# Kernel optimization log

Hardware: AMD Instinct MI355X
Metric: run time of the kernel (lower is better)

Reference implementation:

```python
import jax, jax.numpy as jnp
import numpy as np

B, S, D, H = 4, 2048, 768, 12
DEPTH = D // H


def setup_inputs() -> dict:
    key = jax.random.key(0)
    ks = jax.random.split(key, 8)
    scale = 1.0 / np.sqrt(D)
    return {
        "v": jax.random.normal(ks[0], (B, S, D), jnp.float32),
        "k": jax.random.normal(ks[1], (B, S, D), jnp.float32),
        "q": jax.random.normal(ks[2], (B, S, D), jnp.float32),
        "wq": jax.random.normal(ks[3], (D, D), jnp.float32) * scale,
        "wk": jax.random.normal(ks[4], (D, D), jnp.float32) * scale,
        "wv": jax.random.normal(ks[5], (D, D), jnp.float32) * scale,
        "wo": jax.random.normal(ks[6], (D, D), jnp.float32) * scale,
        "bo": jax.random.normal(ks[7], (D,), jnp.float32) * 0.01,
    }


def _split_heads(x):
    # [B, S, D] -> [B, H, S, depth]
    return x.reshape(B, S, H, DEPTH).transpose(0, 2, 1, 3)


def reference(v, k, q, wq, wk, wv, wo, bo):
    # nn.Linear(bias=False): y = x @ W.T
    qh = _split_heads(q @ wq.T)
    kh = _split_heads(k @ wk.T)
    vh = _split_heads(v @ wv.T)
    # scaled dot-product attention (mask=None)
    logits = jnp.einsum("bhqd,bhkd->bhqk", qh, kh) / jnp.sqrt(
        jnp.asarray(DEPTH, jnp.float32)
    )
    attn = jax.nn.softmax(logits, axis=-1)  # [B, H, Sq, Sk]
    out = jnp.einsum("bhqk,bhkd->bhqd", attn, vh)
    concat = out.transpose(0, 2, 1, 3).reshape(B, S, D)
    return concat @ wo.T + bo
```

## Files before the change

### kernel.cpp

```cpp
#include <hip/hip_runtime.h>
#include <math.h>

#define BB 4
#define SS 2048
#define DD 768
#define HH 12
#define DEPTH 64
#define M_TOTAL (BB * SS)
#define WSZ (DD * DD)

typedef __attribute__((ext_vector_type(8))) short bf16x8;
typedef __attribute__((ext_vector_type(16))) float f32x16;
typedef __attribute__((ext_vector_type(4))) float f32x4;
typedef __attribute__((ext_vector_type(4))) unsigned short us4;

__device__ __forceinline__ unsigned short f2b(float f) {
  union { float f; unsigned int u; } v;
  v.f = f;
  unsigned int u = v.u;
  return (unsigned short)((u + 0x7FFFu + ((u >> 16) & 1u)) >> 16);
}

__device__ __forceinline__ us4 f2b4(float a, float b, float c, float d) {
  us4 t;
  t.x = f2b(a); t.y = f2b(b); t.z = f2b(c); t.w = f2b(d);
  return t;
}

__device__ __forceinline__ float fexp2(float x) {
  return __builtin_amdgcn_exp2f(x);
}

__device__ __forceinline__ void gl16(const void* g, void* l) {
  __builtin_amdgcn_global_load_lds(
      (const __attribute__((address_space(1))) unsigned int*)g,
      (__attribute__((address_space(3))) unsigned int*)l, 16, 0, 0);
}

__global__ __launch_bounds__(256) void prep(
    const float* __restrict__ s0, const float* __restrict__ s1,
    const float* __restrict__ s2, const float* __restrict__ s3,
    const float* __restrict__ s4, const float* __restrict__ s5,
    const float* __restrict__ s6, unsigned short* __restrict__ d0,
    unsigned short* __restrict__ d1, unsigned short* __restrict__ d2,
    unsigned short* __restrict__ d3, unsigned short* __restrict__ d4,
    unsigned short* __restrict__ d5, unsigned short* __restrict__ d6) {
  const float* s;
  unsigned short* d;
  int n;
  switch (blockIdx.y) {
    case 0: s = s0; d = d0; n = M_TOTAL * DD; break;
    case 1: s = s1; d = d1; n = M_TOTAL * DD; break;
    case 2: s = s2; d = d2; n = M_TOTAL * DD; break;
    case 3: s = s3; d = d3; n = WSZ; break;
    case 4: s = s4; d = d4; n = WSZ; break;
    case 5: s = s5; d = d5; n = WSZ; break;
    default: s = s6; d = d6; n = WSZ; break;
  }
  int idx = (blockIdx.x * 256 + threadIdx.x) * 4;
  if (idx >= n) return;
  float4 f = *(const float4*)(s + idx);
  *(us4*)(d + idx) = f2b4(f.x, f.y, f.z, f.w);
}

__global__ __launch_bounds__(256) void proj_qkv(
    const unsigned short* __restrict__ qb, const unsigned short* __restrict__ kb,
    const unsigned short* __restrict__ vb, const unsigned short* __restrict__ wqb,
    const unsigned short* __restrict__ wkb, const unsigned short* __restrict__ wvb,
    unsigned short* __restrict__ QF, unsigned short* __restrict__ KF,
    unsigned short* __restrict__ VF) {
  const int mode = blockIdx.z;
  const unsigned short* X;
  const unsigned short* W;
  if (mode == 0) { X = qb; W = wqb; }
  else if (mode == 1) { X = kb; W = wkb; }
  else { X = vb; W = wvb; }

  __shared__ __align__(16) unsigned short As[128 * 32];
  __shared__ __align__(16) unsigned short Bs[128 * 32];

  const int tid = threadIdx.x;
  const int lane = tid & 63, w_ = tid >> 6;
  const int lr = lane & 15, quad = lane >> 4;
  const int wm = (w_ & 1) * 64, wn = (w_ >> 1) * 64;
  const int m0 = blockIdx.x * 128, n0 = blockIdx.y * 128;
  const int grow = lane >> 2, gcol = (lane & 3) * 8;

  f32x4 acc[4][4];
#pragma unroll
  for (int mt = 0; mt < 4; ++mt)
#pragma unroll
    for (int nt = 0; nt < 4; ++nt) acc[mt][nt] = (f32x4){0.f, 0.f, 0.f, 0.f};

  for (int k0 = 0; k0 < DD; k0 += 32) {
    __syncthreads();
#pragma unroll
    for (int i = 0; i < 2; ++i) {
      int c = 4 * i + w_;
      int row = c * 16 + grow;
      gl16(X + (size_t)(m0 + row) * DD + k0 + gcol, (char*)As + c * 1024);
      gl16(W + (size_t)(n0 + row) * DD + k0 + gcol, (char*)Bs + c * 1024);
    }
    __syncthreads();

    bf16x8 af[4];
#pragma unroll
    for (int mt = 0; mt < 4; ++mt)
      af[mt] = *(const bf16x8*)&As[(wm + 16 * mt + lr) * 32 + 8 * quad];
#pragma unroll
    for (int nt = 0; nt < 4; ++nt) {
      bf16x8 bf = *(const bf16x8*)&Bs[(wn + 16 * nt + lr) * 32 + 8 * quad];
#pragma unroll
      for (int mt = 0; mt < 4; ++mt)
        acc[mt][nt] = __builtin_amdgcn_mfma_f32_16x16x32_bf16(af[mt], bf,
                                                              acc[mt][nt], 0, 0, 0);
    }
  }

  if (mode < 2) {
    unsigned short* O = (mode == 0) ? QF : KF;
    const float osc = (mode == 0) ? 0.18033688011f : 1.0f;
#pragma unroll
    for (int mt = 0; mt < 4; ++mt)
#pragma unroll
      for (int nt = 0; nt < 4; ++nt) {
        int n = n0 + wn + 16 * nt + lr;
        int head = n >> 6, d = n & 63;
        int ks = d >> 4, hbit = (d >> 3) & 1, j = d & 7;
#pragma unroll
        for (int r = 0; r < 4; ++r) {
          int m = m0 + wm + 16 * mt + 4 * quad + r;
          int b_ = m >> 11, s_ = m & 2047;
          int bh = b_ * HH + head;
          int lane2 = hbit * 32 + (s_ & 31);
          size_t off =
              ((((size_t)bh * 64 + (s_ >> 5)) * 4 + ks) * 64 + lane2) * 8 + j;
          O[off] = f2b(acc[mt][nt][r] * osc);
        }
      }
  } else {
#pragma unroll
    for (int mt = 0; mt < 4; ++mt)
#pragma unroll
      for (int nt = 0; nt < 4; ++nt) {
        int n = n0 + wn + 16 * nt + lr;
        int head = n >> 6, d = n & 63;
        int ntv = d >> 5, m32v = d & 31;
        int mb = m0 + wm + 16 * mt + 4 * quad;
        int b_ = mb >> 11, s_ = mb & 2047;
        int bh = b_ * HH + head;
        int sblk = s_ >> 5, ks2 = (s_ >> 4) & 1, hb = (s_ >> 3) & 1, jb = s_ & 7;
        int lane2 = hb * 32 + m32v;
        size_t off =
            (((((size_t)bh * 64 + sblk) * 2 + ntv) * 2 + ks2) * 64 + lane2) * 8 +
            jb;
        *(us4*)&VF[off] =
            f2b4(acc[mt][nt][0], acc[mt][nt][1], acc[mt][nt][2], acc[mt][nt][3]);
      }
  }
}

__global__ __launch_bounds__(256) void attn(
    const unsigned short* __restrict__ QF, const unsigned short* __restrict__ KF,
    const unsigned short* __restrict__ VF, unsigned short* __restrict__ cc) {
  __shared__ __align__(16) char smem[19200];
  unsigned short (*Ps)[32][40] = (unsigned short (*)[32][40])smem;
  float (*Osh)[64][36] = (float (*)[64][36])smem;
  float (*Ls)[2][32] = (float (*)[2][32])(smem + 18432);
  float (*Linv)[32] = (float (*)[32])(smem + 18944);

  const int tid = threadIdx.x;
  const int lane = tid & 63, w_ = tid >> 6;
  const int wq = w_ & 1, wk = w_ >> 1;
  const int m32 = lane & 31, h = lane >> 5;
  const int q0 = blockIdx.x * 64;
  const int bh = blockIdx.y;
  const size_t perbh = (size_t)SS * DEPTH;

  const unsigned short* qfb = QF + (size_t)bh * perbh;
  const unsigned short* kfb = KF + (size_t)bh * perbh;
  const unsigned short* vfb = VF + (size_t)bh * perbh;

  bf16x8 qf[4];
  {
    const int qblk = (q0 >> 5) + wq;
    const unsigned short* p = qfb + (size_t)qblk * 2048 + lane * 8;
#pragma unroll
    for (int ks = 0; ks < 4; ++ks) qf[ks] = *(const bf16x8*)(p + ks * 512);
  }

  f32x16 o[2];
#pragma unroll
  for (int nt = 0; nt < 2; ++nt)
#pragma unroll
    for (int r = 0; r < 16; ++r) o[nt][r] = 0.f;
  float l_lane = 0.f;

  bf16x8 ka[4], vf[4];
  {
    const int sb = wk;
    const unsigned short* kp = kfb + (size_t)sb * 2048 + lane * 8;
    const unsigned short* vp = vfb + (size_t)sb * 2048 + lane * 8;
#pragma unroll
    for (int x = 0; x < 4; ++x) {
      ka[x] = *(const bf16x8*)(kp + x * 512);
      vf[x] = *(const bf16x8*)(vp + x * 512);
    }
  }

  for (int kv0 = 0; kv0 < SS; kv0 += 64) {
    bf16x8 kan[4], vfn[4];
    const bool more = (kv0 + 64 < SS);
    if (more) {
      const int sb = ((kv0 + 64) >> 5) + wk;
      const unsigned short* kp = kfb + (size_t)sb * 2048 + lane * 8;
      const unsigned short* vp = vfb + (size_t)sb * 2048 + lane * 8;
#pragma unroll
      for (int x = 0; x < 4; ++x) {
        kan[x] = *(const bf16x8*)(kp + x * 512);
        vfn[x] = *(const bf16x8*)(vp + x * 512);
      }
    }

    f32x16 st;
#pragma unroll
    for (int r = 0; r < 16; ++r) st[r] = 0.f;
#pragma unroll
    for (int ks = 0; ks < 4; ++ks)
      st = __builtin_amdgcn_mfma_f32_32x32x16_bf16(ka[ks], qf[ks], st, 0, 0, 0);

#pragma unroll
    for (int g = 0; g < 4; ++g) {
      float e0 = fexp2(st[4 * g + 0]);
      float e1 = fexp2(st[4 * g + 1]);
      float e2 = fexp2(st[4 * g + 2]);
      float e3 = fexp2(st[4 * g + 3]);
      l_lane += (e0 + e1) + (e2 + e3);
      *(us4*)&Ps[w_][m32][8 * g + 4 * h] = f2b4(e0, e1, e2, e3);
    }
    asm volatile("s_waitcnt lgkmcnt(0)" ::: "memory");

#pragma unroll
    for (int ks2 = 0; ks2 < 2; ++ks2) {
      bf16x8 pa = *(const bf16x8*)&Ps[w_][m32][16 * ks2 + 8 * h];
      o[0] = __builtin_amdgcn_mfma_f32_32x32x16_bf16(pa, vf[ks2], o[0], 0, 0, 0);
      o[1] = __builtin_amdgcn_mfma_f32_32x32x16_bf16(pa, vf[2 + ks2], o[1], 0, 0, 0);
    }

    if (more) {
#pragma unroll
      for (int x = 0; x < 4; ++x) { ka[x] = kan[x]; vf[x] = vfn[x]; }
    }
  }

  l_lane += __shfl_xor(l_lane, 32);
  if (h == 0) Ls[wq][wk][m32] = l_lane;
  __syncthreads();
  if (wk == 1) {
#pragma unroll
    for (int nt = 0; nt < 2; ++nt)
#pragma unroll
      for (int g = 0; g < 4; ++g) {
        float4 t = make_float4(o[nt][4 * g], o[nt][4 * g + 1], o[nt][4 * g + 2],
                               o[nt][4 * g + 3]);
        *(float4*)&Osh[wq][32 * nt + m32][8 * g + 4 * h] = t;
      }
  } else if (tid < 64) {
    int qq = tid & 31, ww = tid >> 5;
    Linv[ww][qq] = 1.f / (Ls[ww][0][qq] + Ls[ww][1][qq]);
  }
  __syncthreads();
  if (wk == 0) {
    const int b_ = bh / HH, h_ = bh % HH;
#pragma unroll
    for (int g = 0; g < 4; ++g) {
      float4 li = *(const float4*)&Linv[wq][8 * g + 4 * h];
      float lia[4] = {li.x, li.y, li.z, li.w};
#pragma unroll
      for (int nt = 0; nt < 2; ++nt) {
        float4 ot = *(const float4*)&Osh[wq][32 * nt + m32][8 * g + 4 * h];
        float oa[4] = {ot.x, ot.y, ot.z, ot.w};
#pragma unroll
        for (int r = 0; r < 4; ++r) {
          int qg = q0 + 32 * wq + 8 * g + 4 * h + r;
          float val = (o[nt][4 * g + r] + oa[r]) * lia[r];
          cc[((size_t)b_ * SS + qg) * DD + h_ * DEPTH + 32 * nt + m32] = f2b(val);
        }
      }
    }
  }
}

__global__ __launch_bounds__(256) void proj_out(
    const unsigned short* __restrict__ cc, const unsigned short* __restrict__ wob,
    const float* __restrict__ bo, float* __restrict__ out) {
  __shared__ __align__(16) unsigned short As[128 * 32];
  __shared__ __align__(16) unsigned short Bs[128 * 32];

  const int tid = threadIdx.x;
  const int lane = tid & 63, w_ = tid >> 6;
  const int lr = lane & 15, quad = lane >> 4;
  const int wm = (w_ & 1) * 64, wn = (w_ >> 1) * 64;
  const int m0 = blockIdx.x * 128, n0 = blockIdx.y * 128;
  const int grow = lane >> 2, gcol = (lane & 3) * 8;

  f32x4 acc[4][4];
#pragma unroll
  for (int mt = 0; mt < 4; ++mt)
#pragma unroll
    for (int nt = 0; nt < 4; ++nt) acc[mt][nt] = (f32x4){0.f, 0.f, 0.f, 0.f};

  for (int k0 = 0; k0 < DD; k0 += 32) {
    __syncthreads();
#pragma unroll
    for (int i = 0; i < 2; ++i) {
      int c = 4 * i + w_;
      int row = c * 16 + grow;
      gl16(cc + (size_t)(m0 + row) * DD + k0 + gcol, (char*)As + c * 1024);
      gl16(wob + (size_t)(n0 + row) * DD + k0 + gcol, (char*)Bs + c * 1024);
    }
    __syncthreads();

    bf16x8 af[4];
#pragma unroll
    for (int mt = 0; mt < 4; ++mt)
      af[mt] = *(const bf16x8*)&As[(wm + 16 * mt + lr) * 32 + 8 * quad];
#pragma unroll
    for (int nt = 0; nt < 4; ++nt) {
      bf16x8 bf = *(const bf16x8*)&Bs[(wn + 16 * nt + lr) * 32 + 8 * quad];
#pragma unroll
      for (int mt = 0; mt < 4; ++mt)
        acc[mt][nt] = __builtin_amdgcn_mfma_f32_16x16x32_bf16(af[mt], bf,
                                                              acc[mt][nt], 0, 0, 0);
    }
  }

#pragma unroll
  for (int mt = 0; mt < 4; ++mt)
#pragma unroll
    for (int nt = 0; nt < 4; ++nt) {
      int n = n0 + wn + 16 * nt + lr;
      float bias = bo[n];
#pragma unroll
      for (int r = 0; r < 4; ++r) {
        int m = m0 + wm + 16 * mt + 4 * quad + r;
        out[(size_t)m * DD + n] = acc[mt][nt][r] + bias;
      }
    }
}

extern "C" void kernel_launch(void* const* d_in, const int* in_sizes, int n_in,
                              void* d_out, int out_size, void* d_ws,
                              size_t ws_size, hipStream_t stream) {
  const float* v = (const float*)d_in[0];
  const float* k = (const float*)d_in[1];
  const float* q = (const float*)d_in[2];
  const float* wq = (const float*)d_in[3];
  const float* wk = (const float*)d_in[4];
  const float* wv = (const float*)d_in[5];
  const float* wo = (const float*)d_in[6];
  const float* bo = (const float*)d_in[7];
  float* out = (float*)d_out;

  const size_t per = (size_t)BB * HH * SS * DEPTH;
  unsigned short* QF = (unsigned short*)d_ws;
  unsigned short* KF = QF + per;
  unsigned short* VF = KF + per;
  unsigned short* cc = VF + per;
  unsigned short* qb = cc + per;
  unsigned short* kb = qb + per;
  unsigned short* vb = kb + per;
  unsigned short* wqb = vb + per;
  unsigned short* wkb = wqb + WSZ;
  unsigned short* wvb = wkb + WSZ;
  unsigned short* wob = wvb + WSZ;

  dim3 g0(M_TOTAL * DD / 1024, 7);
  prep<<<g0, 256, 0, stream>>>(q, k, v, wq, wk, wv, wo, qb, kb, vb, wqb, wkb,
                               wvb, wob);

  dim3 g1(M_TOTAL / 128, DD / 128, 3);
  proj_qkv<<<g1, 256, 0, stream>>>(qb, kb, vb, wqb, wkb, wvb, QF, KF, VF);

  dim3 g2(SS / 64, BB * HH);
  attn<<<g2, 256, 0, stream>>>(QF, KF, VF, cc);

  dim3 g3(M_TOTAL / 128, DD / 128);
  proj_out<<<g3, 256, 0, stream>>>(cc, wob, bo, out);
}
```

Measured before the change: 285.4 us.

## Stage projection outputs through LDS for coalesced stores; ping-pong KV registers in attention

The QKV projection epilogue now writes its accumulators into a shared-memory tile and then issues coalesced 16-byte stores in the fragment layout the attention kernel expects, replacing scattered 2-byte and 8-byte global writes. In the attention kernel, the next K/V tile is prefetched into one of two register buffers while the other is consumed, instead of copying a prefetch buffer each iteration. The bf16 conversion becomes round-half-up with a byte-permute packing instead of round-to-nearest-even, which changes rounding slightly. The change adds an extra barrier and about 34 KB of LDS in the projection kernel, and more register pressure in attention.

New measurement: 276.1 us. 1.03x faster.

```diff
diff --git a/kernel.cpp b/kernel.cpp
--- a/kernel.cpp
+++ b/kernel.cpp
@@ -13,17 +13,24 @@
 typedef __attribute__((ext_vector_type(16))) float f32x16;
 typedef __attribute__((ext_vector_type(4))) float f32x4;
 typedef __attribute__((ext_vector_type(4))) unsigned short us4;
+typedef __attribute__((ext_vector_type(2))) unsigned int u32x2;
 
 __device__ __forceinline__ unsigned short f2b(float f) {
-  union { float f; unsigned int u; } v;
-  v.f = f;
-  unsigned int u = v.u;
-  return (unsigned short)((u + 0x7FFFu + ((u >> 16) & 1u)) >> 16);
+  unsigned u = __builtin_bit_cast(unsigned, f);
+  return (unsigned short)((u + 0x8000u) >> 16);
+}
+
+__device__ __forceinline__ unsigned pkrnd(float lo, float hi) {
+  unsigned a = __builtin_bit_cast(unsigned, lo) + 0x8000u;
+  unsigned b = __builtin_bit_cast(unsigned, hi) + 0x8000u;
+  return __builtin_amdgcn_perm(b, a, 0x07060302);
 }
 
 __device__ __forceinline__ us4 f2b4(float a, float b, float c, float d) {
+  unsigned lo = pkrnd(a, b), hi = pkrnd(c, d);
   us4 t;
-  t.x = f2b(a); t.y = f2b(b); t.z = f2b(c); t.w = f2b(d);
+  t.x = (unsigned short)lo; t.y = (unsigned short)(lo >> 16);
+  t.z = (unsigned short)hi; t.w = (unsigned short)(hi >> 16);
   return t;
 }
 
@@ -76,8 +83,10 @@
   else if (mode == 1) { X = kb; W = wkb; }
   else { X = vb; W = wvb; }
 
-  __shared__ __align__(16) unsigned short As[128 * 32];
-  __shared__ __align__(16) unsigned short Bs[128 * 32];
+  __shared__ __align__(16) char sm[34816];
+  unsigned short* As = (unsigned short*)sm;
+  unsigned short* Bs = (unsigned short*)(sm + 8192);
+  unsigned short* Ts = (unsigned short*)sm;
 
   const int tid = threadIdx.x;
   const int lane = tid & 63, w_ = tid >> 6;
@@ -117,48 +126,63 @@
     }
   }
 
+  __syncthreads();
+
+  const int b_ = m0 >> 11;
+  const int hbase = n0 >> 6;
+  const int sgbase = (m0 & 2047) >> 5;
+
   if (mode < 2) {
+    const float osc = (mode == 0) ? 0.18033688011f : 1.0f;
+#pragma unroll
+    for (int mt = 0; mt < 4; ++mt)
+#pragma unroll
+      for (int nt = 0; nt < 4; ++nt) {
+        int n = wn + 16 * nt + lr;
+        int mb = wm + 16 * mt + 4 * quad;
+#pragma unroll
+        for (int r = 0; r < 4; ++r)
+          Ts[(mb + r) * 136 + n] = f2b(acc[mt][nt][r] * osc);
+      }
+    __syncthreads();
     unsigned short* O = (mode == 0) ? QF : KF;
-    const float osc = (mode == 0) ? 0.18033688011f : 1.0f;
+    const int ks = tid >> 6, lane2 = tid & 63;
+    const int mrow = lane2 & 31, hb = lane2 >> 5;
+#pragma unroll
+    for (int c = 0; c < 8; ++c) {
+      int hl = c >> 2, sblk = c & 3;
+      int bh = b_ * HH + hbase + hl;
+      bf16x8 vv = *(const bf16x8*)&Ts[(sblk * 32 + mrow) * 136 + hl * 64 +
+                                      ks * 16 + hb * 8];
+      *(bf16x8*)(O + ((size_t)bh * 64 + sgbase + sblk) * 2048 + tid * 8) = vv;
+    }
+  } else {
 #pragma unroll
     for (int mt = 0; mt < 4; ++mt)
 #pragma unroll
       for (int nt = 0; nt < 4; ++nt) {
-        int n = n0 + wn + 16 * nt + lr;
-        int head = n >> 6, d = n & 63;
-        int ks = d >> 4, hbit = (d >> 3) & 1, j = d & 7;
-#pragma unroll
-        for (int r = 0; r < 4; ++r) {
-          int m = m0 + wm + 16 * mt + 4 * quad + r;
-          int b_ = m >> 11, s_ = m & 2047;
-          int bh = b_ * HH + head;
-          int lane2 = hbit * 32 + (s_ & 31);
-          size_t off =
-              ((((size_t)bh * 64 + (s_ >> 5)) * 4 + ks) * 64 + lane2) * 8 + j;
-          O[off] = f2b(acc[mt][nt][r] * osc);
-        }
-      }
-  } else {
-#pragma unroll
-    for (int mt = 0; mt < 4; ++mt)
-#pragma unroll
-      for (int nt = 0; nt < 4; ++nt) {
-        int n = n0 + wn + 16 * nt + lr;
-        int head = n >> 6, d = n & 63;
-        int ntv = d >> 5, m32v = d & 31;
-        int mb = m0 + wm + 16 * mt + 4 * quad;
-        int b_ = mb >> 11, s_ = mb & 2047;
-        int bh = b_ * HH + head;
-        int sblk = s_ >> 5, ks2 = (s_ >> 4) & 1, hb = (s_ >> 3) & 1, jb = s_ & 7;
-        int lane2 = hb * 32 + m32v;
-        size_t off =
-            (((((size_t)bh * 64 + sblk) * 2 + ntv) * 2 + ks2) * 64 + lane2) * 8 +
-            jb;
-        *(us4*)&VF[off] =
+        int n = wn + 16 * nt + lr;
+        int mb = wm + 16 * mt + 4 * quad;
+        *(us4*)&Ts[n * 136 + mb] =
             f2b4(acc[mt][nt][0], acc[mt][nt][1], acc[mt][nt][2], acc[mt][nt][3]);
       }
-  }
-}
+    __syncthreads();
+    const int ntv = tid >> 7, ks2 = (tid >> 6) & 1, lane2 = tid & 63;
+#pragma unroll
+    for (int c = 0; c < 8; ++c) {
+      int hl = c >> 2, sblk = c & 3;
+      int bh = b_ * HH + hbase + hl;
+      bf16x8 vv = *(const bf16x8*)&Ts[(hl * 64 + ntv * 32 + (lane2 & 31)) * 136 +
+                                      sblk * 32 + ks2 * 16 + (lane2 >> 5) * 8];
+      *(bf16x8*)(VF + ((size_t)bh * 64 + sgbase + sblk) * 2048 + tid * 8) = vv;
+    }
+  }
+}
+
+struct KV {
+  bf16x8 k[4];
+  bf16x8 v[4];
+};
 
 __global__ __launch_bounds__(256) void attn(
     const unsigned short* __restrict__ QF, const unsigned short* __restrict__ KF,
@@ -178,13 +202,12 @@
   const size_t perbh = (size_t)SS * DEPTH;
 
   const unsigned short* qfb = QF + (size_t)bh * perbh;
-  const unsigned short* kfb = KF + (size_t)bh * perbh;
-  const unsigned short* vfb = VF + (size_t)bh * perbh;
+  const unsigned short* kfb = KF + (size_t)bh * perbh + (size_t)wk * 2048 + lane * 8;
+  const unsigned short* vfb = VF + (size_t)bh * perbh + (size_t)wk * 2048 + lane * 8;
 
   bf16x8 qf[4];
   {
-    const int qblk = (q0 >> 5) + wq;
-    const unsigned short* p = qfb + (size_t)qblk * 2048 + lane * 8;
+    const unsigned short* p = qfb + (size_t)((q0 >> 5) + wq) * 2048 + lane * 8;
 #pragma unroll
     for (int ks = 0; ks < 4; ++ks) qf[ks] = *(const bf16x8*)(p + ks * 512);
   }
@@ -196,61 +219,48 @@
     for (int r = 0; r < 16; ++r) o[nt][r] = 0.f;
   float l_lane = 0.f;
 
-  bf16x8 ka[4], vf[4];
-  {
-    const int sb = wk;
-    const unsigned short* kp = kfb + (size_t)sb * 2048 + lane * 8;
-    const unsigned short* vp = vfb + (size_t)sb * 2048 + lane * 8;
-#pragma unroll
-    for (int x = 0; x < 4; ++x) {
-      ka[x] = *(const bf16x8*)(kp + x * 512);
-      vf[x] = *(const bf16x8*)(vp + x * 512);
-    }
-  }
-
-  for (int kv0 = 0; kv0 < SS; kv0 += 64) {
-    bf16x8 kan[4], vfn[4];
-    const bool more = (kv0 + 64 < SS);
-    if (more) {
-      const int sb = ((kv0 + 64) >> 5) + wk;
-      const unsigned short* kp = kfb + (size_t)sb * 2048 + lane * 8;
-      const unsigned short* vp = vfb + (size_t)sb * 2048 + lane * 8;
-#pragma unroll
-      for (int x = 0; x < 4; ++x) {
-        kan[x] = *(const bf16x8*)(kp + x * 512);
-        vfn[x] = *(const bf16x8*)(vp + x * 512);
-      }
-    }
-
-    f32x16 st;
-#pragma unroll
-    for (int r = 0; r < 16; ++r) st[r] = 0.f;
-#pragma unroll
-    for (int ks = 0; ks < 4; ++ks)
-      st = __builtin_amdgcn_mfma_f32_32x32x16_bf16(ka[ks], qf[ks], st, 0, 0, 0);
-
-#pragma unroll
-    for (int g = 0; g < 4; ++g) {
-      float e0 = fexp2(st[4 * g + 0]);
-      float e1 = fexp2(st[4 * g + 1]);
-      float e2 = fexp2(st[4 * g + 2]);
-      float e3 = fexp2(st[4 * g + 3]);
-      l_lane += (e0 + e1) + (e2 + e3);
-      *(us4*)&Ps[w_][m32][8 * g + 4 * h] = f2b4(e0, e1, e2, e3);
-    }
-    asm volatile("s_waitcnt lgkmcnt(0)" ::: "memory");
-
-#pragma unroll
-    for (int ks2 = 0; ks2 < 2; ++ks2) {
-      bf16x8 pa = *(const bf16x8*)&Ps[w_][m32][16 * ks2 + 8 * h];
-      o[0] = __builtin_amdgcn_mfma_f32_32x32x16_bf16(pa, vf[ks2], o[0], 0, 0, 0);
-      o[1] = __builtin_amdgcn_mfma_f32_32x32x16_bf16(pa, vf[2 + ks2], o[1], 0, 0, 0);
-    }
-
-    if (more) {
-#pragma unroll
-      for (int x = 0; x < 4; ++x) { ka[x] = kan[x]; vf[x] = vfn[x]; }
-    }
+#define LOADKV(tile, dst)                                                    \
+  do {                                                                       \
+    const unsigned short* kp_ = kfb + (size_t)(tile) * 4096;                 \
+    const unsigned short* vp_ = vfb + (size_t)(tile) * 4096;                 \
+    _Pragma("unroll") for (int x_ = 0; x_ < 4; ++x_) {                       \
+      (dst).k[x_] = *(const bf16x8*)(kp_ + x_ * 512);                        \
+      (dst).v[x_] = *(const bf16x8*)(vp_ + x_ * 512);                        \
+    }                                                                        \
+  } while (0)
+
+#define TILECOMP(kv)                                                         \
+  do {                                                                       \
+    f32x16 st;                                                               \
+    _Pragma("unroll") for (int r_ = 0; r_ < 16; ++r_) st[r_] = 0.f;          \
+    _Pragma("unroll") for (int ks_ = 0; ks_ < 4; ++ks_)                      \
+        st = __builtin_amdgcn_mfma_f32_32x32x16_bf16((kv).k[ks_], qf[ks_],   \
+                                                     st, 0, 0, 0);           \
+    _Pragma("unroll") for (int g_ = 0; g_ < 4; ++g_) {                       \
+      float e0 = fexp2(st[4 * g_ + 0]), e1 = fexp2(st[4 * g_ + 1]);          \
+      float e2 = fexp2(st[4 * g_ + 2]), e3 = fexp2(st[4 * g_ + 3]);          \
+      l_lane += (e0 + e1) + (e2 + e3);                                       \
+      u32x2 pp;                                                              \
+      pp.x = pkrnd(e0, e1);                                                  \
+      pp.y = pkrnd(e2, e3);                                                  \
+      *(u32x2*)&Ps[w_][m32][8 * g_ + 4 * h] = pp;                            \
+    }                                                                        \
+    _Pragma("unroll") for (int ks2_ = 0; ks2_ < 2; ++ks2_) {                 \
+      bf16x8 pa = *(const bf16x8*)&Ps[w_][m32][16 * ks2_ + 8 * h];           \
+      o[0] = __builtin_amdgcn_mfma_f32_32x32x16_bf16(pa, (kv).v[ks2_],       \
+                                                     o[0], 0, 0, 0);         \
+      o[1] = __builtin_amdgcn_mfma_f32_32x32x16_bf16(pa, (kv).v[2 + ks2_],   \
+                                                     o[1], 0, 0, 0);         \
+    }                                                                        \
+  } while (0)
+
+  KV b0, b1;
+  LOADKV(0, b0);
+  for (int t = 0; t < 32; t += 2) {
+    LOADKV(t + 1, b1);
+    TILECOMP(b0);
+    if (t + 2 < 32) LOADKV(t + 2, b0);
+    TILECOMP(b1);
   }
 
   l_lane += __shfl_xor(l_lane, 32);
```
